# Kernel optimization log

Measured on AMD Instinct MI355X. Metric: run time of the kernel, lower is better.

## Reference

```python
import jax, jax.numpy as jnp
import numpy as np


def setup_inputs() -> dict:
    key = jax.random.key(0)
    k1, k2 = jax.random.split(key)
    B, C = 65536, 1000
    output = jax.random.normal(k1, (B, C), dtype=jnp.float32)
    target = jax.random.uniform(k2, (B, C), dtype=jnp.float32)  # soft labels in [0,1)
    return {"output": output, "target": target}


def _multivector_ce(output, target, size_average=True):
    # For each row: positives P = {t>0.5}, negatives N = {t<=0.5}.
    # Original loop computes, per positive p:
    #   loss_p = sum_{j in N u {p}} -t_j * log_softmax_{N u {p}}(o)_j
    # which factors through shared negative-set statistics:
    #   LSE_p = log( sum_{j in N} exp(o_j) + exp(o_p) )
    #   loss_p = (Tneg + t_p) * LSE_p - Aneg - t_p * o_p
    # with Tneg = sum_N t_j, Aneg = sum_N t_j * o_j.
    neg = target <= 0.5                                   # [B, C] bool
    m = jnp.max(output, axis=1, keepdims=True)            # [B, 1] stability shift
    e = jnp.exp(output - m)                               # [B, C]
    zero = jnp.zeros((), dtype=output.dtype)
    Sneg = jnp.sum(jnp.where(neg, e, zero), axis=1, keepdims=True)              # [B, 1]
    Tneg = jnp.sum(jnp.where(neg, target, zero), axis=1, keepdims=True)         # [B, 1]
    Aneg = jnp.sum(jnp.where(neg, target * output, zero), axis=1, keepdims=True)

    lse_p = m + jnp.log(Sneg + e)                         # [B, C], LSE of N u {p} per candidate p
    loss_p = (Tneg + target) * lse_p - Aneg - target * output   # [B, C]

    pos = ~neg
    n_pos = jnp.sum(pos, axis=1)                          # [B] int
    pos_loss = jnp.sum(jnp.where(pos, loss_p, zero), axis=1)    # [B]

    # Fallback when a row has no positives: loss over negatives only.
    lse_neg = (m + jnp.log(Sneg))[:, 0]                   # [B]
    fallback = Tneg[:, 0] * lse_neg - Aneg[:, 0]          # [B]

    denom = jnp.maximum(n_pos, 1).astype(output.dtype)
    row_loss = jnp.where(n_pos > 0, pos_loss / denom, fallback)  # [B]

    total = jnp.sum(row_loss)
    if size_average:
        return total / output.shape[0]
    return total


def reference(output, target):
    return _multivector_ce(output, target, size_average=True)
```

## Files before the change

### kernel.cpp

```cpp
#include <hip/hip_runtime.h>
#include <math.h>

#define C_DIM 1000
#define NV4   (C_DIM / 4)
#define WPB   4
#define RPW   4
#define PAD_O (-100.0f)

__device__ __forceinline__ float wave_sum(float v) {
#pragma unroll
    for (int off = 32; off > 0; off >>= 1)
        v += __shfl_xor(v, off, 64);
    return v;
}

__device__ __forceinline__ void wave_sum4(float& a, float& b, float& c, float& d) {
#pragma unroll
    for (int off = 32; off > 0; off >>= 1) {
        const float ax = __shfl_xor(a, off, 64);
        const float bx = __shfl_xor(b, off, 64);
        const float cx = __shfl_xor(c, off, 64);
        const float dx = __shfl_xor(d, off, 64);
        a += ax; b += bx; c += cx; d += dx;
    }
}

__device__ __forceinline__ void load_row(
    const float* __restrict__ outp, const float* __restrict__ tgtp,
    int row, int lane, float o[16], float t[16])
{
    const float4* orow = reinterpret_cast<const float4*>(outp + (size_t)row * C_DIM);
    const float4* trow = reinterpret_cast<const float4*>(tgtp + (size_t)row * C_DIM);
#pragma unroll
    for (int it = 0; it < 4; ++it) {
        const int j = lane + 64 * it;
        if (j < NV4) {
            const float4 ov = orow[j];
            const float4 tv = trow[j];
            o[4 * it + 0] = ov.x; o[4 * it + 1] = ov.y;
            o[4 * it + 2] = ov.z; o[4 * it + 3] = ov.w;
            t[4 * it + 0] = tv.x; t[4 * it + 1] = tv.y;
            t[4 * it + 2] = tv.z; t[4 * it + 3] = tv.w;
        } else {
#pragma unroll
            for (int q = 0; q < 4; ++q) {
                o[4 * it + q] = PAD_O;
                t[4 * it + q] = 0.0f;
            }
        }
    }
}

__global__ __launch_bounds__(256) void mvce_rows(
    const float* __restrict__ outp, const float* __restrict__ tgtp,
    float* __restrict__ partial)
{
    const int lane = threadIdx.x & 63;
    const int wave = threadIdx.x >> 6;
    const int wgid = blockIdx.x * WPB + wave;
    const int row0 = wgid * RPW;

    float oA[16], tA[16], oB[16], tB[16];
    load_row(outp, tgtp, row0, lane, oA, tA);

    float wsum_lane = 0.0f;

#pragma unroll
    for (int r = 0; r < RPW; ++r) {
        if (r + 1 < RPW)
            load_row(outp, tgtp, row0 + r + 1, lane, oB, tB);

        float e[16];
        float S = 0.f, T = 0.f, A = 0.f, P = 0.f;
#pragma unroll
        for (int k = 0; k < 16; ++k) {
            e[k] = __expf(oA[k]);
            const bool neg = (tA[k] <= 0.5f);
            const float tn = neg ? tA[k] : 0.0f;
            S += neg ? e[k] : 0.0f;
            T += tn;
            A  = fmaf(tn, oA[k], A);
            P += neg ? 0.0f : 1.0f;
        }
        wave_sum4(S, T, A, P);

        float L = 0.f;
#pragma unroll
        for (int k = 0; k < 16; ++k) {
            const float lse = __logf(S + e[k]);
            const float b   = fmaf(tA[k], oA[k], A);
            const float c   = fmaf(T + tA[k], lse, -b);
            L += (tA[k] > 0.5f) ? c : 0.0f;
        }

        if (P > 0.5f) {
            wsum_lane += L / P;
        } else if (lane == 0) {
            wsum_lane += fmaf(T, __logf(S), -A);
        }

        if (r + 1 < RPW) {
#pragma unroll
            for (int k = 0; k < 16; ++k) { oA[k] = oB[k]; tA[k] = tB[k]; }
        }
    }

    const float wsum = wave_sum(wsum_lane);

    __shared__ float ls[WPB];
    if (lane == 0) ls[wave] = wsum;
    __syncthreads();
    if (threadIdx.x == 0)
        partial[blockIdx.x] = (ls[0] + ls[1]) + (ls[2] + ls[3]);
}

__global__ __launch_bounds__(256) void mvce_reduce(
    const float* __restrict__ partial, int n4, float inv_b, float* __restrict__ out)
{
    const float4* p4 = reinterpret_cast<const float4*>(partial);
    float s = 0.f;
#pragma unroll 4
    for (int i = threadIdx.x; i < n4; i += 256) {
        const float4 v = p4[i];
        s += (v.x + v.y) + (v.z + v.w);
    }
    s = wave_sum(s);
    __shared__ float ls[4];
    const int lane = threadIdx.x & 63;
    const int wave = threadIdx.x >> 6;
    if (lane == 0) ls[wave] = s;
    __syncthreads();
    if (threadIdx.x == 0) out[0] = ((ls[0] + ls[1]) + (ls[2] + ls[3])) * inv_b;
}

extern "C" void kernel_launch(void* const* d_in, const int* in_sizes, int n_in,
                              void* d_out, int out_size, void* d_ws, size_t ws_size,
                              hipStream_t stream) {
    const float* outp = (const float*)d_in[0];
    const float* tgtp = (const float*)d_in[1];
    const int Bn = in_sizes[0] / C_DIM;
    const int nblocks = Bn / (WPB * RPW);
    float* partial = (float*)d_ws;

    mvce_rows<<<nblocks, 256, 0, stream>>>(outp, tgtp, partial);
    mvce_reduce<<<1, 256, 0, stream>>>(partial, nblocks / 4, 1.0f / (float)Bn,
                                       (float*)d_out);
}
```

Before: 495.1 us.

## Process two rows per wave with all loads issued upfront and merged reductions

Each wave now handles two rows instead of four, issuing all eight float4 loads for both rows before any compute, with a scheduling barrier that keeps the loads grouped. The two rows' statistics are reduced together in one 8-wide shuffle reduction, and launch bounds request 4 blocks per SM. This doubles the grid size and raises memory-level parallelism in place of the old software-pipelined row loop. The trade-off is more blocks and partials, which means more reduce-kernel work and more registers live per thread.

```diff
diff --git a/kernel.cpp b/kernel.cpp
--- a/kernel.cpp
+++ b/kernel.cpp
@@ -4,7 +4,6 @@
 #define C_DIM 1000
 #define NV4   (C_DIM / 4)
 #define WPB   4
-#define RPW   4
 #define PAD_O (-100.0f)
 
 __device__ __forceinline__ float wave_sum(float v) {
@@ -14,97 +13,88 @@
     return v;
 }
 
-__device__ __forceinline__ void wave_sum4(float& a, float& b, float& c, float& d) {
+__device__ __forceinline__ void wave_sum8(float v[8]) {
 #pragma unroll
     for (int off = 32; off > 0; off >>= 1) {
-        const float ax = __shfl_xor(a, off, 64);
-        const float bx = __shfl_xor(b, off, 64);
-        const float cx = __shfl_xor(c, off, 64);
-        const float dx = __shfl_xor(d, off, 64);
-        a += ax; b += bx; c += cx; d += dx;
+        float x[8];
+#pragma unroll
+        for (int i = 0; i < 8; ++i) x[i] = __shfl_xor(v[i], off, 64);
+#pragma unroll
+        for (int i = 0; i < 8; ++i) v[i] += x[i];
     }
 }
 
-__device__ __forceinline__ void load_row(
-    const float* __restrict__ outp, const float* __restrict__ tgtp,
-    int row, int lane, float o[16], float t[16])
-{
-    const float4* orow = reinterpret_cast<const float4*>(outp + (size_t)row * C_DIM);
-    const float4* trow = reinterpret_cast<const float4*>(tgtp + (size_t)row * C_DIM);
-#pragma unroll
-    for (int it = 0; it < 4; ++it) {
-        const int j = lane + 64 * it;
-        if (j < NV4) {
-            const float4 ov = orow[j];
-            const float4 tv = trow[j];
-            o[4 * it + 0] = ov.x; o[4 * it + 1] = ov.y;
-            o[4 * it + 2] = ov.z; o[4 * it + 3] = ov.w;
-            t[4 * it + 0] = tv.x; t[4 * it + 1] = tv.y;
-            t[4 * it + 2] = tv.z; t[4 * it + 3] = tv.w;
-        } else {
-#pragma unroll
-            for (int q = 0; q < 4; ++q) {
-                o[4 * it + q] = PAD_O;
-                t[4 * it + q] = 0.0f;
-            }
-        }
-    }
-}
-
-__global__ __launch_bounds__(256) void mvce_rows(
+__global__ __launch_bounds__(256, 4) void mvce_rows(
     const float* __restrict__ outp, const float* __restrict__ tgtp,
     float* __restrict__ partial)
 {
     const int lane = threadIdx.x & 63;
     const int wave = threadIdx.x >> 6;
-    const int wgid = blockIdx.x * WPB + wave;
-    const int row0 = wgid * RPW;
+    const int row0 = (blockIdx.x * WPB + wave) * 2;
 
-    float oA[16], tA[16], oB[16], tB[16];
-    load_row(outp, tgtp, row0, lane, oA, tA);
+    const float4* __restrict__ o0 = reinterpret_cast<const float4*>(outp + (size_t)row0 * C_DIM);
+    const float4* __restrict__ t0 = reinterpret_cast<const float4*>(tgtp + (size_t)row0 * C_DIM);
+    const float4* __restrict__ o1 = o0 + NV4;
+    const float4* __restrict__ t1 = t0 + NV4;
 
-    float wsum_lane = 0.0f;
+    float o[2][16], t[2][16];
+#pragma unroll
+    for (int it = 0; it < 4; ++it) {
+        const int j = lane + 64 * it;
+        if (j < NV4) {
+            const float4 a0 = o0[j]; const float4 b0 = t0[j];
+            const float4 a1 = o1[j]; const float4 b1 = t1[j];
+            o[0][4*it+0]=a0.x; o[0][4*it+1]=a0.y; o[0][4*it+2]=a0.z; o[0][4*it+3]=a0.w;
+            t[0][4*it+0]=b0.x; t[0][4*it+1]=b0.y; t[0][4*it+2]=b0.z; t[0][4*it+3]=b0.w;
+            o[1][4*it+0]=a1.x; o[1][4*it+1]=a1.y; o[1][4*it+2]=a1.z; o[1][4*it+3]=a1.w;
+            t[1][4*it+0]=b1.x; t[1][4*it+1]=b1.y; t[1][4*it+2]=b1.z; t[1][4*it+3]=b1.w;
+        } else {
+#pragma unroll
+            for (int r = 0; r < 2; ++r)
+#pragma unroll
+                for (int q = 0; q < 4; ++q) { o[r][4*it+q] = PAD_O; t[r][4*it+q] = 0.0f; }
+        }
+    }
+    __builtin_amdgcn_sched_barrier(0);
 
+    float e[2][16];
+    float st[8] = {0,0,0,0, 0,0,0,0};
 #pragma unroll
-    for (int r = 0; r < RPW; ++r) {
-        if (r + 1 < RPW)
-            load_row(outp, tgtp, row0 + r + 1, lane, oB, tB);
+    for (int k = 0; k < 16; ++k) {
+#pragma unroll
+        for (int r = 0; r < 2; ++r) {
+            const float ok = o[r][k], tk = t[r][k];
+            e[r][k] = __expf(ok);
+            const bool neg = (tk <= 0.5f);
+            const float tn = neg ? tk : 0.0f;
+            st[4*r+0] += neg ? e[r][k] : 0.0f;
+            st[4*r+1] += tn;
+            st[4*r+2]  = fmaf(tn, ok, st[4*r+2]);
+            st[4*r+3] += neg ? 0.0f : 1.0f;
+        }
+    }
+    wave_sum8(st);
 
-        float e[16];
-        float S = 0.f, T = 0.f, A = 0.f, P = 0.f;
+    float L[2] = {0.0f, 0.0f};
 #pragma unroll
-        for (int k = 0; k < 16; ++k) {
-            e[k] = __expf(oA[k]);
-            const bool neg = (tA[k] <= 0.5f);
-            const float tn = neg ? tA[k] : 0.0f;
-            S += neg ? e[k] : 0.0f;
-            T += tn;
-            A  = fmaf(tn, oA[k], A);
-            P += neg ? 0.0f : 1.0f;
-        }
-        wave_sum4(S, T, A, P);
-
-        float L = 0.f;
+    for (int k = 0; k < 16; ++k) {
 #pragma unroll
-        for (int k = 0; k < 16; ++k) {
-            const float lse = __logf(S + e[k]);
-            const float b   = fmaf(tA[k], oA[k], A);
-            const float c   = fmaf(T + tA[k], lse, -b);
-            L += (tA[k] > 0.5f) ? c : 0.0f;
-        }
-
-        if (P > 0.5f) {
-            wsum_lane += L / P;
-        } else if (lane == 0) {
-            wsum_lane += fmaf(T, __logf(S), -A);
-        }
-
-        if (r + 1 < RPW) {
-#pragma unroll
-            for (int k = 0; k < 16; ++k) { oA[k] = oB[k]; tA[k] = tB[k]; }
+        for (int r = 0; r < 2; ++r) {
+            const float ok = o[r][k], tk = t[r][k];
+            const float lse = __logf(st[4*r+0] + e[r][k]);
+            const float b   = fmaf(tk, ok, st[4*r+2]);
+            const float c   = fmaf(st[4*r+1] + tk, lse, -b);
+            L[r] += (tk > 0.5f) ? c : 0.0f;
         }
     }
 
+    float wsum_lane = 0.0f;
+#pragma unroll
+    for (int r = 0; r < 2; ++r) {
+        const float S = st[4*r+0], T = st[4*r+1], A = st[4*r+2], P = st[4*r+3];
+        if (P > 0.5f)       wsum_lane += L[r] / P;
+        else if (lane == 0) wsum_lane += fmaf(T, __logf(S), -A);
+    }
     const float wsum = wave_sum(wsum_lane);
 
     __shared__ float ls[WPB];
@@ -139,7 +129,7 @@
     const float* outp = (const float*)d_in[0];
     const float* tgtp = (const float*)d_in[1];
     const int Bn = in_sizes[0] / C_DIM;
-    const int nblocks = Bn / (WPB * RPW);
+    const int nblocks = Bn / (WPB * 2);
     float* partial = (float*)d_ws;
 
     mvce_rows<<<nblocks, 256, 0, stream>>>(outp, tgtp, partial);
```

Result: no change. 491.5 us (-0.7%).

## Stream rows via global_load_lds into double-buffered LDS, drop block reduce

Applied to the files above, without the earlier changes.

Replaces the register-based float4 prefetch with direct global-to-LDS async DMA into a per-wave double buffer, waiting on vmcnt before consuming each row. Values are reread from LDS in the second pass, and exp is recomputed instead of held in registers, which lowers register pressure. Rows per wave double, and each wave writes its own partial, so the block-level shared-memory sync goes away. The cost is 64KB of LDS per block, which can limit occupancy, plus extra LDS reads and exp evaluations.

```diff
diff --git a/kernel.cpp b/kernel.cpp
--- a/kernel.cpp
+++ b/kernel.cpp
@@ -2,10 +2,20 @@
 #include <math.h>
 
 #define C_DIM 1000
-#define NV4   (C_DIM / 4)
+#define NV4   250
 #define WPB   4
-#define RPW   4
+#define RPW   8
+#define CHUNK 256
+#define ROWF  1024
 #define PAD_O (-100.0f)
+
+#define GLOBAL_AS __attribute__((address_space(1)))
+#define LDS_AS    __attribute__((address_space(3)))
+
+__device__ __forceinline__ void dma16(const float* g, float* l) {
+    __builtin_amdgcn_global_load_lds((const GLOBAL_AS void*)g, (LDS_AS void*)l,
+                                     16, 0, 0);
+}
 
 __device__ __forceinline__ float wave_sum(float v) {
 #pragma unroll
@@ -25,29 +35,18 @@
     }
 }
 
-__device__ __forceinline__ void load_row(
-    const float* __restrict__ outp, const float* __restrict__ tgtp,
-    int row, int lane, float o[16], float t[16])
-{
-    const float4* orow = reinterpret_cast<const float4*>(outp + (size_t)row * C_DIM);
-    const float4* trow = reinterpret_cast<const float4*>(tgtp + (size_t)row * C_DIM);
+__device__ __forceinline__ void issue_row(const float* __restrict__ outp,
+                                          const float* __restrict__ tgtp,
+                                          int row, int lane,
+                                          float* lo, float* lt) {
+    const float* orow = outp + (size_t)row * C_DIM;
+    const float* trow = tgtp + (size_t)row * C_DIM;
 #pragma unroll
     for (int it = 0; it < 4; ++it) {
-        const int j = lane + 64 * it;
-        if (j < NV4) {
-            const float4 ov = orow[j];
-            const float4 tv = trow[j];
-            o[4 * it + 0] = ov.x; o[4 * it + 1] = ov.y;
-            o[4 * it + 2] = ov.z; o[4 * it + 3] = ov.w;
-            t[4 * it + 0] = tv.x; t[4 * it + 1] = tv.y;
-            t[4 * it + 2] = tv.z; t[4 * it + 3] = tv.w;
-        } else {
-#pragma unroll
-            for (int q = 0; q < 4; ++q) {
-                o[4 * it + q] = PAD_O;
-                t[4 * it + q] = 0.0f;
-            }
-        }
+        const int j  = lane + 64 * it;
+        const int jj = (j < NV4) ? (j * 4) : 0;
+        dma16(orow + jj, lo + it * CHUNK);
+        dma16(trow + jj, lt + it * CHUNK);
     }
 }
 
@@ -55,63 +54,81 @@
     const float* __restrict__ outp, const float* __restrict__ tgtp,
     float* __restrict__ partial)
 {
+    __shared__ float lds[WPB][2][2][ROWF];
+
     const int lane = threadIdx.x & 63;
     const int wave = threadIdx.x >> 6;
     const int wgid = blockIdx.x * WPB + wave;
     const int row0 = wgid * RPW;
 
-    float oA[16], tA[16], oB[16], tB[16];
-    load_row(outp, tgtp, row0, lane, oA, tA);
+    issue_row(outp, tgtp, row0, lane, lds[wave][0][0], lds[wave][0][1]);
 
     float wsum_lane = 0.0f;
 
 #pragma unroll
     for (int r = 0; r < RPW; ++r) {
+        const int buf = r & 1;
         if (r + 1 < RPW)
-            load_row(outp, tgtp, row0 + r + 1, lane, oB, tB);
+            issue_row(outp, tgtp, row0 + r + 1, lane,
+                      lds[wave][buf ^ 1][0], lds[wave][buf ^ 1][1]);
 
-        float e[16];
+        if (r + 1 < RPW) __builtin_amdgcn_s_waitcnt(0x0F78);
+        else             __builtin_amdgcn_s_waitcnt(0x0F70);
+        __builtin_amdgcn_sched_barrier(0);
+
+        const float4* lo4 = reinterpret_cast<const float4*>(lds[wave][buf][0]);
+        const float4* lt4 = reinterpret_cast<const float4*>(lds[wave][buf][1]);
+
         float S = 0.f, T = 0.f, A = 0.f, P = 0.f;
 #pragma unroll
-        for (int k = 0; k < 16; ++k) {
-            e[k] = __expf(oA[k]);
-            const bool neg = (tA[k] <= 0.5f);
-            const float tn = neg ? tA[k] : 0.0f;
-            S += neg ? e[k] : 0.0f;
-            T += tn;
-            A  = fmaf(tn, oA[k], A);
-            P += neg ? 0.0f : 1.0f;
+        for (int it = 0; it < 4; ++it) {
+            float4 ov = lo4[lane + 64 * it];
+            float4 tv = lt4[lane + 64 * it];
+            if (it == 3 && lane >= 58) {
+                ov = make_float4(PAD_O, PAD_O, PAD_O, PAD_O);
+                tv = make_float4(0.f, 0.f, 0.f, 0.f);
+            }
+            const float oo[4] = {ov.x, ov.y, ov.z, ov.w};
+            const float tt[4] = {tv.x, tv.y, tv.z, tv.w};
+#pragma unroll
+            for (int q = 0; q < 4; ++q) {
+                const float e   = __expf(oo[q]);
+                const bool  neg = (tt[q] <= 0.5f);
+                const float tn  = neg ? tt[q] : 0.0f;
+                S += neg ? e : 0.0f;
+                T += tn;
+                A  = fmaf(tn, oo[q], A);
+                P += neg ? 0.0f : 1.0f;
+            }
         }
         wave_sum4(S, T, A, P);
 
         float L = 0.f;
 #pragma unroll
-        for (int k = 0; k < 16; ++k) {
-            const float lse = __logf(S + e[k]);
-            const float b   = fmaf(tA[k], oA[k], A);
-            const float c   = fmaf(T + tA[k], lse, -b);
-            L += (tA[k] > 0.5f) ? c : 0.0f;
+        for (int it = 0; it < 4; ++it) {
+            float4 ov = lo4[lane + 64 * it];
+            float4 tv = lt4[lane + 64 * it];
+            if (it == 3 && lane >= 58) {
+                ov = make_float4(PAD_O, PAD_O, PAD_O, PAD_O);
+                tv = make_float4(0.f, 0.f, 0.f, 0.f);
+            }
+            const float oo[4] = {ov.x, ov.y, ov.z, ov.w};
+            const float tt[4] = {tv.x, tv.y, tv.z, tv.w};
+#pragma unroll
+            for (int q = 0; q < 4; ++q) {
+                const float lse = __logf(S + __expf(oo[q]));
+                const float b   = fmaf(tt[q], oo[q], A);
+                const float c   = fmaf(T + tt[q], lse, -b);
+                L += (tt[q] > 0.5f) ? c : 0.0f;
+            }
         }
 
-        if (P > 0.5f) {
-            wsum_lane += L / P;
-        } else if (lane == 0) {
-            wsum_lane += fmaf(T, __logf(S), -A);
-        }
-
-        if (r + 1 < RPW) {
-#pragma unroll
-            for (int k = 0; k < 16; ++k) { oA[k] = oB[k]; tA[k] = tB[k]; }
-        }
+        if (P > 0.5f)       wsum_lane += L / P;
+        else if (lane == 0) wsum_lane += fmaf(T, __logf(S), -A);
     }
 
     const float wsum = wave_sum(wsum_lane);
-
-    __shared__ float ls[WPB];
-    if (lane == 0) ls[wave] = wsum;
-    __syncthreads();
-    if (threadIdx.x == 0)
-        partial[blockIdx.x] = (ls[0] + ls[1]) + (ls[2] + ls[3]);
+    if (lane == 0) partial[wgid] = wsum;
 }
 
 __global__ __launch_bounds__(256) void mvce_reduce(
@@ -140,9 +157,10 @@
     const float* tgtp = (const float*)d_in[1];
     const int Bn = in_sizes[0] / C_DIM;
     const int nblocks = Bn / (WPB * RPW);
+    const int nwaves  = nblocks * WPB;
     float* partial = (float*)d_ws;
 
     mvce_rows<<<nblocks, 256, 0, stream>>>(outp, tgtp, partial);
-    mvce_reduce<<<1, 256, 0, stream>>>(partial, nblocks / 4, 1.0f / (float)Bn,
+    mvce_reduce<<<1, 256, 0, stream>>>(partial, nwaves / 4, 1.0f / (float)Bn,
                                        (float*)d_out);
 }
```

After: 502.9 us. Within noise of the previous version (+1.6%).
